# Kernel optimization log

Measured on AMD Instinct MI355X. Metric: run time of the kernel, lower is better.

The kernel has to match this reference:

```python
import jax, jax.numpy as jnp
import numpy as np

# Module hyperparameters (from init_kwargs)
START = 0.0      # lower distance cutoff
STOP = 5.0       # radius_graph cutoff r
K = 32           # max_num_neighbors
N_ATOMS = 16384
N_GRAPHS = 64
BOX = 30.0       # box edge length (Angstrom) -> realistic density for r=5 cutoff


def setup_inputs() -> dict:
    key = jax.random.key(0)
    k1, k2 = jax.random.split(key)
    pos = jax.random.uniform(k1, (N_ATOMS, 3), dtype=jnp.float32) * BOX
    batch = jnp.sort(jax.random.randint(k2, (N_ATOMS,), 0, N_GRAPHS)).astype(jnp.int64)
    return {"pos": pos, "batch": batch}


def reference(pos, batch):
    """radius_graph (loop=False) + edge vectors/norms + lower-cutoff mask.

    Because jit requires static shapes, the variable-length edge list of the
    original is returned in padded form: edge_index [2, N*K], edge_weight [N*K],
    edge_vec [N*K, 3], plus a boolean validity mask [N*K]. Valid entries match
    the original (edge_index, edge_weight, edge_vec) after compaction.
    """
    N = pos.shape[0]
    # Pairwise squared distances via the Gram trick: [N, N], memory-bound.
    sq = jnp.sum(pos * pos, axis=-1)
    d2 = sq[:, None] + sq[None, :] - 2.0 * (pos @ pos.T)
    idx = jnp.arange(N)
    valid = (batch[:, None] == batch[None, :]) \
            & (idx[:, None] != idx[None, :]) \
            & (d2 <= STOP * STOP)
    d2m = jnp.where(valid, d2, jnp.inf)
    # Up to K nearest neighbors within the radius per node.
    neg_d2, nbr = jax.lax.top_k(-d2m, K)          # [N, K]
    nbr_valid = neg_d2 > -jnp.inf                  # in-radius, same-graph, non-self
    nbr = jnp.where(nbr_valid, nbr, idx[:, None])  # pad with self (vec = 0)
    # edge_vec = pos[center] - pos[neighbor]  (pos[edge_index[0]] - pos[edge_index[1]])
    edge_vec = pos[:, None, :] - pos[nbr]          # [N, K, 3]
    sqd = jnp.sum(edge_vec * edge_vec, axis=-1)
    w = jnp.where(nbr_valid, jnp.sqrt(jnp.where(nbr_valid, sqd, 1.0)), 0.0)
    lower = nbr_valid & (w >= START)               # lower cutoff mask
    src = jnp.broadcast_to(idx[:, None], (N, K))
    edge_index = jnp.stack([src.reshape(-1), nbr.reshape(-1)])  # [2, N*K]
    mask = lower.reshape(-1)
    edge_weight = jnp.where(lower, w, 0.0).reshape(-1)
    edge_vec = jnp.where(lower[..., None], edge_vec, 0.0).reshape(-1, 3)
    return edge_index, edge_weight, edge_vec, mask
```

## Files before the change

### kernel.cpp

```cpp
#include <hip/hip_runtime.h>
#include <math.h>

#define KNBR 32
#define STOP2 25.0
#define BAND 1.0e-3f
#define CAND_CAP 1024
#define CAP 64
#define WPB 8
#define APW 2
#define APB (WPB*APW)

__global__ __launch_bounds__(WPB * 64)
void radius_graph_knn(const float* __restrict__ pos,
                      const int* __restrict__ batch,
                      float* __restrict__ out, int n) {
    __shared__ float spos[3 * CAND_CAP];
    __shared__ int   sbatch[CAND_CAP];
    __shared__ int   jbuf[WPB][APW][CAP];
    __shared__ int   win[WPB][KNBR];

    const int tid  = threadIdx.x;
    const int lane = tid & 63;
    const int w    = tid >> 6;
    const int i0   = blockIdx.x * APB;

    const int bFirst = batch[i0];
    const int bLast  = batch[min(i0 + APB - 1, n - 1)];
    const int nchunks = (n + 63) >> 6;
    const int c0 = i0 >> 6;
    const int cw = c0 - 32 + lane;
    bool rel = false;
    if (cw >= 0 && cw < nchunks) {
        const int s = batch[cw << 6];
        const int e = batch[min(n - 1, (cw << 6) + 63)];
        rel = (s <= bLast) && (e >= bFirst);
    }
    const unsigned long long cm = __ballot(rel);
    const int cLo = c0 - 32 + (int)__builtin_ctzll(cm);
    const int cHi = c0 - 32 + (63 - (int)__builtin_clzll(cm));
    const int base = cLo << 6;
    int stagedN = min(n, (cHi + 1) << 6) - base;
    if (stagedN > CAND_CAP) stagedN = CAND_CAP;

    {
        const float4* __restrict__ src = (const float4*)(pos + 3 * (size_t)base);
        float4* __restrict__ dst = (float4*)spos;
        const int nvec = (3 * stagedN) >> 2;
        for (int t = tid; t < nvec; t += WPB * 64) dst[t] = src[t];
        for (int t = tid; t < stagedN; t += WPB * 64) sbatch[t] = batch[base + t];
    }
    __syncthreads();

    int ia[APW]; int ba[APW];
    float xa[APW], ya[APW], za[APW];
    #pragma unroll
    for (int a = 0; a < APW; ++a) {
        const int i = min(i0 + w * APW + a, n - 1);
        ia[a] = i;
        const int si = i - base;
        xa[a] = spos[3 * si]; ya[a] = spos[3 * si + 1]; za[a] = spos[3 * si + 2];
        ba[a] = sbatch[si];
    }

    int cnt[APW] = {0, 0};
    for (int t0 = 0; t0 < stagedN; t0 += 64) {
        const int t = t0 + lane;
        const int tc = min(t, stagedN - 1);
        const float xj = spos[3 * tc], yj = spos[3 * tc + 1], zj = spos[3 * tc + 2];
        const int bj = sbatch[tc];
        const int j = base + tc;
        #pragma unroll
        for (int a = 0; a < APW; ++a) {
            const float dx = xa[a] - xj, dy = ya[a] - yj, dz = za[a] - zj;
            const float d2 = dx * dx + dy * dy + dz * dz;
            const bool valid = (t < stagedN) & (j != ia[a]) & (bj == ba[a]) &
                               (d2 <= 25.0f + BAND);
            const unsigned long long m = __ballot(valid);
            const int p = cnt[a] + __popcll(m & ((1ULL << lane) - 1ULL));
            if (valid && p < CAP) jbuf[w][a][p] = tc;
            cnt[a] += __popcll(m);
        }
    }

    const long long NK = (long long)n * KNBR;
    float* row0 = out;
    float* row1 = out + NK;
    float* wgt  = out + 2 * NK;
    float* vec  = out + 3 * NK;
    float* msk  = out + 6 * NK;

    #pragma unroll
    for (int a = 0; a < APW; ++a) {
        const int count = min(cnt[a], CAP);
        double d2e = 1e300;
        int jmine = 0x7fffffff, slot = 0;
        bool valid = false;
        if (lane < count) {
            slot = jbuf[w][a][lane];
            const double dx = (double)xa[a] - (double)spos[3 * slot];
            const double dy = (double)ya[a] - (double)spos[3 * slot + 1];
            const double dz = (double)za[a] - (double)spos[3 * slot + 2];
            d2e = dx * dx + dy * dy + dz * dz;
            jmine = base + slot;
            valid = (d2e <= STOP2);
        }
        const unsigned long long vm = __ballot(valid);
        int nsel = __popcll(vm);
        if (nsel > KNBR) nsel = KNBR;
        int rank = 0;
        for (int s = 0; s < count; ++s) {
            const double ds = __shfl(d2e, s);
            const int    js = __shfl(jmine, s);
            const bool   vs = (vm >> s) & 1ULL;
            rank += (vs && (ds < d2e || (ds == d2e && js < jmine))) ? 1 : 0;
        }
        if (valid && rank < KNBR) win[w][rank] = slot;

        const int i = ia[a];
        const long long obase = (long long)i * KNBR;
        if (lane < KNBR) {
            const int s = lane;
            const bool v = (s < nsel);
            const int sl = v ? win[w][s] : (i - base);
            const int j = base + sl;
            const float vx = xa[a] - spos[3 * sl];
            const float vy = ya[a] - spos[3 * sl + 1];
            const float vz = za[a] - spos[3 * sl + 2];
            const float ww = v ? sqrtf(vx * vx + vy * vy + vz * vz) : 0.0f;
            row0[obase + s] = (float)i;
            row1[obase + s] = (float)j;
            wgt[obase + s]  = ww;
            vec[3 * (obase + s) + 0] = v ? vx : 0.0f;
            vec[3 * (obase + s) + 1] = v ? vy : 0.0f;
            vec[3 * (obase + s) + 2] = v ? vz : 0.0f;
            msk[obase + s]  = v ? 1.0f : 0.0f;
        }
    }
}

extern "C" void kernel_launch(void* const* d_in, const int* in_sizes, int n_in,
                              void* d_out, int out_size, void* d_ws, size_t ws_size,
                              hipStream_t stream) {
    const float* pos   = (const float*)d_in[0];
    const int*   batch = (const int*)d_in[1];
    float* out = (float*)d_out;
    int n = in_sizes[1];

    const int block = WPB * 64;
    const int grid = (n + APB - 1) / APB;
    radius_graph_knn<<<grid, block, 0, stream>>>(pos, batch, out, n);
}
```

Baseline: 69.57 us.

## Drop LDS candidate staging; read positions directly from global per wave

Removes the block-wide shared-memory staging of candidate positions and batch ids, along with its __syncthreads. Each wave now computes its own candidate window and reads positions straight from global memory, relying on cache. The block shrinks to 4 waves with an occupancy hint. The output phase is restructured so both atoms per wave write their 32 slots in a single pass using all 64 lanes. This cuts LDS usage and staging latency but turns candidate reads into repeated global loads and drops the CAND_CAP clamp on the candidate range.

```diff
diff --git a/kernel.cpp b/kernel.cpp
--- a/kernel.cpp
+++ b/kernel.cpp
@@ -4,30 +4,37 @@
 #define KNBR 32
 #define STOP2 25.0
 #define BAND 1.0e-3f
-#define CAND_CAP 1024
 #define CAP 64
-#define WPB 8
+#define WPB 4
 #define APW 2
 #define APB (WPB*APW)
 
-__global__ __launch_bounds__(WPB * 64)
+__global__ __launch_bounds__(WPB * 64, 8)
 void radius_graph_knn(const float* __restrict__ pos,
                       const int* __restrict__ batch,
                       float* __restrict__ out, int n) {
-    __shared__ float spos[3 * CAND_CAP];
-    __shared__ int   sbatch[CAND_CAP];
-    __shared__ int   jbuf[WPB][APW][CAP];
-    __shared__ int   win[WPB][KNBR];
+    __shared__ int jbuf[WPB][APW][CAP];
+    __shared__ int win[WPB][APW][KNBR];
 
     const int tid  = threadIdx.x;
     const int lane = tid & 63;
     const int w    = tid >> 6;
-    const int i0   = blockIdx.x * APB;
+    const int i0w  = (blockIdx.x * WPB + w) * APW;
 
-    const int bFirst = batch[i0];
-    const int bLast  = batch[min(i0 + APB - 1, n - 1)];
+    int ia[APW]; int ba[APW];
+    float xa[APW], ya[APW], za[APW];
+    #pragma unroll
+    for (int a = 0; a < APW; ++a) {
+        const int i = min(i0w + a, n - 1);
+        ia[a] = i;
+        xa[a] = pos[3 * i]; ya[a] = pos[3 * i + 1]; za[a] = pos[3 * i + 2];
+        ba[a] = batch[i];
+    }
+    const int bFirst = ba[0];
+    const int bLast  = ba[APW - 1];
+
     const int nchunks = (n + 63) >> 6;
-    const int c0 = i0 >> 6;
+    const int c0 = i0w >> 6;
     const int cw = c0 - 32 + lane;
     bool rel = false;
     if (cw >= 0 && cw < nchunks) {
@@ -39,36 +46,15 @@
     const int cLo = c0 - 32 + (int)__builtin_ctzll(cm);
     const int cHi = c0 - 32 + (63 - (int)__builtin_clzll(cm));
     const int base = cLo << 6;
-    int stagedN = min(n, (cHi + 1) << 6) - base;
-    if (stagedN > CAND_CAP) stagedN = CAND_CAP;
-
-    {
-        const float4* __restrict__ src = (const float4*)(pos + 3 * (size_t)base);
-        float4* __restrict__ dst = (float4*)spos;
-        const int nvec = (3 * stagedN) >> 2;
-        for (int t = tid; t < nvec; t += WPB * 64) dst[t] = src[t];
-        for (int t = tid; t < stagedN; t += WPB * 64) sbatch[t] = batch[base + t];
-    }
-    __syncthreads();
-
-    int ia[APW]; int ba[APW];
-    float xa[APW], ya[APW], za[APW];
-    #pragma unroll
-    for (int a = 0; a < APW; ++a) {
-        const int i = min(i0 + w * APW + a, n - 1);
-        ia[a] = i;
-        const int si = i - base;
-        xa[a] = spos[3 * si]; ya[a] = spos[3 * si + 1]; za[a] = spos[3 * si + 2];
-        ba[a] = sbatch[si];
-    }
+    const int stagedN = min(n, (cHi + 1) << 6) - base;
 
     int cnt[APW] = {0, 0};
     for (int t0 = 0; t0 < stagedN; t0 += 64) {
         const int t = t0 + lane;
         const int tc = min(t, stagedN - 1);
-        const float xj = spos[3 * tc], yj = spos[3 * tc + 1], zj = spos[3 * tc + 2];
-        const int bj = sbatch[tc];
         const int j = base + tc;
+        const float xj = pos[3 * j], yj = pos[3 * j + 1], zj = pos[3 * j + 2];
+        const int bj = batch[j];
         #pragma unroll
         for (int a = 0; a < APW; ++a) {
             const float dx = xa[a] - xj, dy = ya[a] - yj, dz = za[a] - zj;
@@ -77,9 +63,39 @@
                                (d2 <= 25.0f + BAND);
             const unsigned long long m = __ballot(valid);
             const int p = cnt[a] + __popcll(m & ((1ULL << lane) - 1ULL));
-            if (valid && p < CAP) jbuf[w][a][p] = tc;
+            if (valid && p < CAP) jbuf[w][a][p] = j;
             cnt[a] += __popcll(m);
         }
+    }
+
+    int nsel[APW];
+    #pragma unroll
+    for (int a = 0; a < APW; ++a) {
+        const int count = min(cnt[a], CAP);
+        double d2e = 1e300;
+        int jmine = 0x7fffffff;
+        bool valid = false;
+        if (lane < count) {
+            const int j = jbuf[w][a][lane];
+            const double dx = (double)xa[a] - (double)pos[3 * j];
+            const double dy = (double)ya[a] - (double)pos[3 * j + 1];
+            const double dz = (double)za[a] - (double)pos[3 * j + 2];
+            d2e = dx * dx + dy * dy + dz * dz;
+            jmine = j;
+            valid = (d2e <= STOP2);
+        }
+        const unsigned long long vm = __ballot(valid);
+        int ns = __popcll(vm);
+        if (ns > KNBR) ns = KNBR;
+        nsel[a] = ns;
+        int rank = 0;
+        for (int s = 0; s < count; ++s) {
+            const double ds = __shfl(d2e, s);
+            const int    js = __shfl(jmine, s);
+            const bool   vs = (vm >> s) & 1ULL;
+            rank += (vs && (ds < d2e || (ds == d2e && js < jmine))) ? 1 : 0;
+        }
+        if (valid && rank < KNBR) win[w][a][rank] = jmine;
     }
 
     const long long NK = (long long)n * KNBR;
@@ -89,53 +105,27 @@
     float* vec  = out + 3 * NK;
     float* msk  = out + 6 * NK;
 
-    #pragma unroll
-    for (int a = 0; a < APW; ++a) {
-        const int count = min(cnt[a], CAP);
-        double d2e = 1e300;
-        int jmine = 0x7fffffff, slot = 0;
-        bool valid = false;
-        if (lane < count) {
-            slot = jbuf[w][a][lane];
-            const double dx = (double)xa[a] - (double)spos[3 * slot];
-            const double dy = (double)ya[a] - (double)spos[3 * slot + 1];
-            const double dz = (double)za[a] - (double)spos[3 * slot + 2];
-            d2e = dx * dx + dy * dy + dz * dz;
-            jmine = base + slot;
-            valid = (d2e <= STOP2);
-        }
-        const unsigned long long vm = __ballot(valid);
-        int nsel = __popcll(vm);
-        if (nsel > KNBR) nsel = KNBR;
-        int rank = 0;
-        for (int s = 0; s < count; ++s) {
-            const double ds = __shfl(d2e, s);
-            const int    js = __shfl(jmine, s);
-            const bool   vs = (vm >> s) & 1ULL;
-            rank += (vs && (ds < d2e || (ds == d2e && js < jmine))) ? 1 : 0;
-        }
-        if (valid && rank < KNBR) win[w][rank] = slot;
-
-        const int i = ia[a];
-        const long long obase = (long long)i * KNBR;
-        if (lane < KNBR) {
-            const int s = lane;
-            const bool v = (s < nsel);
-            const int sl = v ? win[w][s] : (i - base);
-            const int j = base + sl;
-            const float vx = xa[a] - spos[3 * sl];
-            const float vy = ya[a] - spos[3 * sl + 1];
-            const float vz = za[a] - spos[3 * sl + 2];
-            const float ww = v ? sqrtf(vx * vx + vy * vy + vz * vz) : 0.0f;
-            row0[obase + s] = (float)i;
-            row1[obase + s] = (float)j;
-            wgt[obase + s]  = ww;
-            vec[3 * (obase + s) + 0] = v ? vx : 0.0f;
-            vec[3 * (obase + s) + 1] = v ? vy : 0.0f;
-            vec[3 * (obase + s) + 2] = v ? vz : 0.0f;
-            msk[obase + s]  = v ? 1.0f : 0.0f;
-        }
-    }
+    const int a = lane >> 5;
+    const int s = lane & 31;
+    const int   i  = a ? ia[1] : ia[0];
+    const float xi = a ? xa[1] : xa[0];
+    const float yi = a ? ya[1] : ya[0];
+    const float zi = a ? za[1] : za[0];
+    const int   ns = a ? nsel[1] : nsel[0];
+    const bool v = s < ns;
+    const int j = v ? win[w][a][s] : i;
+    const float vx = xi - pos[3 * j];
+    const float vy = yi - pos[3 * j + 1];
+    const float vz = zi - pos[3 * j + 2];
+    const float ww = v ? sqrtf(vx * vx + vy * vy + vz * vz) : 0.0f;
+    const long long o = (long long)i * KNBR + s;
+    row0[o] = (float)i;
+    row1[o] = (float)j;
+    wgt[o]  = ww;
+    vec[3 * o + 0] = v ? vx : 0.0f;
+    vec[3 * o + 1] = v ? vy : 0.0f;
+    vec[3 * o + 2] = v ? vz : 0.0f;
+    msk[o]  = v ? 1.0f : 0.0f;
 }
 
 extern "C" void kernel_launch(void* const* d_in, const int* in_sizes, int n_in,
```

Result: no change. 69.17 us (-0.6%).
